# Kernel tuning notes

Hardware: AMD Instinct MI355X
Metric: run time of the kernel (lower is better)

The kernel has to match this reference:

```python
import jax, jax.numpy as jnp
import numpy as np

B, NPG, DEG = 512, 128, 16          # graphs, nodes/graph, out-degree
N = B * NPG                          # 65536 nodes
E = N * DEG                          # 1048576 edges
IN_DIM, HID, HEADS = 11, 32, 4
K1 = int(np.ceil(0.8 * NPG))         # 103 nodes/graph after pool1
K2 = int(np.ceil(0.8 * K1))          # 83 nodes/graph after pool2


def gat_conv(x, src, dst, mask, W, a_s, a_d, b, n_nodes):
    # PyG GATConv (concat=True, add_self_loops=True, eval mode -> no dropout)
    xp = (x @ W).reshape(n_nodes, HEADS, HID)            # [N,H,C]
    as_ = jnp.einsum('nhc,hc->nh', xp, a_s)
    ad_ = jnp.einsum('nhc,hc->nh', xp, a_d)
    loop = jnp.arange(n_nodes)
    s = jnp.concatenate([src, loop])
    d = jnp.concatenate([dst, loop])
    m = jnp.concatenate([mask, jnp.ones(n_nodes, bool)])
    logit = jax.nn.leaky_relu(as_[s] + ad_[d], 0.2)      # [E+N,H]
    logit = jnp.where(m[:, None], logit, -1e9)
    mx = jax.ops.segment_max(logit, d, num_segments=n_nodes)
    ex = jnp.exp(logit - mx[d]) * m[:, None]
    den = jax.ops.segment_sum(ex, d, num_segments=n_nodes)
    alpha = ex / (den[d] + 1e-16)                        # segment softmax over dst
    out = jax.ops.segment_sum(alpha[:, :, None] * xp[s], d, num_segments=n_nodes)
    return out.reshape(n_nodes, HEADS * HID) + b


def topk_pool(x, src, dst, mask, w, npg, k):
    # PyG TopKPooling: score = tanh((x*w).sum(-1)/||w||); keep top ceil(ratio*n) per graph
    nb = x.shape[0] // npg
    score = jnp.tanh((x @ w) / jnp.linalg.norm(w))
    vals, idx = jax.lax.top_k(score.reshape(nb, npg), k)  # [B,k]
    perm = (idx + (jnp.arange(nb) * npg)[:, None]).reshape(-1)
    x_new = x[perm] * vals.reshape(-1, 1)
    remap = jnp.full(nb * npg, -1).at[perm].set(jnp.arange(nb * k))
    ns, nd = remap[src], remap[dst]
    m = mask & (ns >= 0) & (nd >= 0)
    return x_new, jnp.where(m, ns, 0), jnp.where(m, nd, 0), m


def setup_inputs():
    key = jax.random.key(0)
    ks = jax.random.split(key, 24)
    s = 0.05
    x = jax.random.normal(ks[0], (N, IN_DIM), jnp.float32)
    src = jnp.repeat(jnp.arange(N), DEG)
    dst = (src // NPG) * NPG + jax.random.randint(ks[1], (E,), 0, NPG)
    edge_index = jnp.stack([src, dst])
    edge_attr = jax.random.normal(ks[2], (E, 4), jnp.float32)
    batch = jnp.repeat(jnp.arange(B), NPG)
    p = dict(
        W_g1=jax.random.normal(ks[3], (IN_DIM, HEADS * HID), jnp.float32) * s,
        att_src1=jax.random.normal(ks[4], (HEADS, HID), jnp.float32) * s,
        att_dst1=jax.random.normal(ks[5], (HEADS, HID), jnp.float32) * s,
        b_g1=jnp.zeros((HEADS * HID,), jnp.float32),
        W_t1=jax.random.normal(ks[6], (HEADS * HID, HID), jnp.float32) * s,
        b_t1=jnp.zeros((HID,), jnp.float32),
        pool_w1=jax.random.normal(ks[7], (HID,), jnp.float32) * s,
        W_g2=jax.random.normal(ks[8], (HID, HEADS * HID), jnp.float32) * s,
        att_src2=jax.random.normal(ks[9], (HEADS, HID), jnp.float32) * s,
        att_dst2=jax.random.normal(ks[10], (HEADS, HID), jnp.float32) * s,
        b_g2=jnp.zeros((HEADS * HID,), jnp.float32),
        W_t2=jax.random.normal(ks[11], (HEADS * HID, HID), jnp.float32) * s,
        b_t2=jnp.zeros((HID,), jnp.float32),
        pool_w2=jax.random.normal(ks[12], (HID,), jnp.float32) * s,
        W_l1=jax.random.normal(ks[13], (2 * HID, 256), jnp.float32) * s,
        b_l1=jnp.zeros((256,), jnp.float32),
        W_l2=jax.random.normal(ks[14], (256, 1024), jnp.float32) * s,
        b_l2=jnp.zeros((1024,), jnp.float32),
        W_l3=jax.random.normal(ks[15], (1024, 1), jnp.float32) * s,
        b_l3=jnp.zeros((1,), jnp.float32),
    )
    return dict(x=x, edge_index=edge_index, edge_attr=edge_attr, batch=batch, **p)


def reference(x, edge_index, edge_attr, batch,
              W_g1, att_src1, att_dst1, b_g1, W_t1, b_t1, pool_w1,
              W_g2, att_src2, att_dst2, b_g2, W_t2, b_t2, pool_w2,
              W_l1, b_l1, W_l2, b_l2, W_l3, b_l3):
    # edge_attr is ignored (GATConv built without edge_dim); batch is implicit
    # in the fixed equal-size graph layout.  Eval mode -> dropout disabled.
    src, dst = edge_index[0], edge_index[1]
    mask = jnp.ones(E, bool)
    h = jax.nn.relu(gat_conv(x, src, dst, mask, W_g1, att_src1, att_dst1, b_g1, N))
    h = h @ W_t1 + b_t1
    h, src, dst, mask = topk_pool(h, src, dst, mask, pool_w1, NPG, K1)
    h1 = h.reshape(B, K1, HID)
    g1 = jnp.concatenate([h1.max(1), h1.mean(1)], axis=1)   # [B, 2*HID]
    h = jax.nn.relu(gat_conv(h, src, dst, mask, W_g2, att_src2, att_dst2, b_g2, B * K1))
    h = h @ W_t2 + b_t2
    h, src, dst, mask = topk_pool(h, src, dst, mask, pool_w2, K1, K2)
    h2 = h.reshape(B, K2, HID)
    g2 = jnp.concatenate([h2.max(1), h2.mean(1)], axis=1)
    g = g1 + g2
    g = jax.nn.relu(g @ W_l1 + b_l1)
    g = jax.nn.relu(g @ W_l2 + b_l2)
    return g @ W_l3 + b_l3                                   # [B,1]
```

## Files before the change

kernel.cpp:

```cpp
#include <hip/hip_runtime.h>
#include <math.h>

constexpr int NPGc  = 128;
constexpr int NG    = 512;
constexpr int EPGc  = 2048;
constexpr int ETOT  = 1048576;
constexpr int IND   = 11;
constexpr int HIDc  = 32;
constexpr int FD    = 128;
constexpr int K1c   = 103;
constexpr int K2c   = 83;
constexpr int NN    = NG * NPGc;
constexpr int N2c   = NG * K1c;

__device__ __forceinline__ float lrelu(float x){ return fmaxf(x, 0.2f*x); }

__device__ __forceinline__ unsigned flipF(float f){
    unsigned u = __float_as_uint(f);
    return u ^ (unsigned)(((int)u >> 31) | 0x80000000);
}
__device__ __forceinline__ float unflipF(unsigned u){
    unsigned m = ((u >> 31) - 1u) | 0x80000000u;
    return __uint_as_float(u ^ m);
}

template<int KIN>
__device__ void foldDev(const float* __restrict__ Wg, const float* __restrict__ avs,
                        const float* __restrict__ avd, float* __restrict__ S, float* __restrict__ D, int t)
{
    if (t < KIN * 4) {
        int k = t >> 2, h = t & 3;
        float s = 0.f, d = 0.f;
        for (int j = 0; j < HIDc; j++) {
            float w = Wg[k*FD + h*HIDc + j];
            s = fmaf(w, avs[h*HIDc + j], s);
            d = fmaf(w, avd[h*HIDc + j], d);
        }
        S[t] = s; D[t] = d;
    }
}
__global__ void k_fold2(const float* W1, const float* s1, const float* d1, float* S1, float* D1,
                        const float* W2, const float* s2, const float* d2, float* S2, float* D2)
{
    if (blockIdx.x == 0) foldDev<IND>(W1, s1, d1, S1, D1, threadIdx.x);
    else                 foldDev<HIDc>(W2, s2, d2, S2, D2, threadIdx.x);
}

template<int NNODE, int KIN, bool REMAP>
__global__ __launch_bounds__(256) void k_gat(
    const float* __restrict__ xin, const float* __restrict__ Wg,
    const float* __restrict__ WsS, const float* __restrict__ WsD,
    const int* __restrict__ ei, const int* __restrict__ rankv,
    const float* __restrict__ bias, float* __restrict__ outp)
{
    int g = blockIdx.x, h = blockIdx.y, t = threadIdx.x;
    __shared__ __align__(16) float xpL[NNODE * 36];
    __shared__ float wE[EPGc];
    __shared__ unsigned char bucket[EPGc];
    __shared__ float asL[NNODE], adL[NNODE], mLn[NNODE], selfW[NNODE], sDen[NNODE];
    __shared__ unsigned maxAsU[NNODE];
    __shared__ int cnt[128], offA[130], curA[128];
    __shared__ float WL[KIN * 32];
    __shared__ float WsSL[KIN], WsDL[KIN];
    __shared__ float bL[32];
    __shared__ signed char rmap[NPGc];

    constexpr bool STAGE = (NNODE * KIN <= EPGc);
    float* xL = wE;

    for (int i = t; i < KIN * 32; i += 256) { int k = i >> 5, c = i & 31; WL[i] = Wg[k*FD + h*32 + c]; }
    if (t < KIN) { WsSL[t] = WsS[t*4 + h]; WsDL[t] = WsD[t*4 + h]; }
    if (t < 32) bL[t] = bias[h*32 + t];
    if (t < 128) cnt[t] = 0;
    if constexpr (REMAP) { if (t < NPGc) rmap[t] = (signed char)rankv[g*NPGc + t]; }
    if constexpr (STAGE) {
        const float* xg = xin + (size_t)g * NNODE * KIN;
        for (int i = t; i < NNODE * KIN; i += 256) xL[i] = xg[i];
    }
    __syncthreads();

    for (int p = t; p < NNODE * 32; p += 256) {
        int n = p >> 5, c = p & 31;
        float acc = 0.f;
        if constexpr (STAGE) {
            const float* xr = xL + n * KIN;
            #pragma unroll
            for (int k = 0; k < KIN; k++) acc = fmaf(xr[k], WL[k*32 + c], acc);
        } else {
            const float* xr = xin + (size_t)(g * NNODE + n) * KIN;
            #pragma unroll
            for (int k = 0; k < KIN; k++) acc = fmaf(xr[k], WL[k*32 + c], acc);
        }
        xpL[n*36 + c] = acc;
    }
    for (int n = t; n < NNODE; n += 256) {
        float s = 0.f, d = 0.f;
        if constexpr (STAGE) {
            const float* xr = xL + n * KIN;
            #pragma unroll
            for (int k = 0; k < KIN; k++) { float xv = xr[k]; s = fmaf(xv, WsSL[k], s); d = fmaf(xv, WsDL[k], d); }
        } else {
            const float* xr = xin + (size_t)(g * NNODE + n) * KIN;
            #pragma unroll
            for (int k = 0; k < KIN; k++) { float xv = xr[k]; s = fmaf(xv, WsSL[k], s); d = fmaf(xv, WsDL[k], d); }
        }
        asL[n] = s; adL[n] = d; maxAsU[n] = flipF(s);
    }
    __syncthreads();

    const int* dstG = ei + ETOT + g * EPGc;
    for (int e = t; e < EPGc; e += 256) {
        int dO = dstG[e] - g * NPGc, s0 = e >> 4;
        if constexpr (REMAP) {
            int sn = rmap[s0], dn = rmap[dO];
            if (sn >= 0 && dn >= 0) { atomicAdd(&cnt[dn], 1); atomicMax(&maxAsU[dn], flipF(asL[sn])); }
        } else {
            atomicAdd(&cnt[dO], 1); atomicMax(&maxAsU[dO], flipF(asL[s0]));
        }
    }
    __syncthreads();

    if (t < 64) {
        int c0 = cnt[2*t], c1 = cnt[2*t + 1], ps = c0 + c1, P = ps;
        #pragma unroll
        for (int dlt = 1; dlt < 64; dlt <<= 1) { int v = __shfl_up(P, dlt); if (t >= dlt) P += v; }
        int E0 = P - ps;
        offA[2*t] = E0; offA[2*t + 1] = E0 + c0;
        curA[2*t] = E0; curA[2*t + 1] = E0 + c0;
        if (t == 63) offA[128] = P;
    } else if (t < 64 + NNODE) {
        int n = t - 64;
        float m = lrelu(unflipF(maxAsU[n]) + adL[n]);
        mLn[n] = m;
        float ws = expf(lrelu(asL[n] + adL[n]) - m);
        selfW[n] = ws; sDen[n] = ws;
    }
    __syncthreads();

    for (int e = t; e < EPGc; e += 256) {
        int dO = dstG[e] - g * NPGc, s0 = e >> 4;
        int sn, dn; bool ok;
        if constexpr (REMAP) { sn = rmap[s0]; dn = rmap[dO]; ok = (sn >= 0 && dn >= 0); }
        else                 { sn = s0; dn = dO; ok = true; }
        if (ok) {
            float w = expf(lrelu(asL[sn] + adL[dn]) - mLn[dn]);
            int pos = atomicAdd(&curA[dn], 1);
            bucket[pos] = (unsigned char)sn; wE[pos] = w;
            atomicAdd(&sDen[dn], w);
        }
    }
    __syncthreads();

    const float4* X4 = (const float4*)xpL;
    for (int p = t; p < NNODE * 8; p += 256) {
        int n = p >> 3, c4 = p & 7;
        float w0 = selfW[n];
        float4 v = X4[n*9 + c4];
        float4 acc; acc.x = w0*v.x; acc.y = w0*v.y; acc.z = w0*v.z; acc.w = w0*v.w;
        int lo = offA[n], hi = offA[n + 1];
        for (int i = lo; i < hi; i++) {
            int sc = bucket[i]; float w = wE[i];
            float4 u = X4[sc*9 + c4];
            acc.x = fmaf(w, u.x, acc.x); acc.y = fmaf(w, u.y, acc.y);
            acc.z = fmaf(w, u.z, acc.z); acc.w = fmaf(w, u.w, acc.w);
        }
        float inv = 1.f / (sDen[n] + 1e-16f);
        float4 r;
        r.x = fmaxf(fmaf(acc.x, inv, bL[c4*4 + 0]), 0.f);
        r.y = fmaxf(fmaf(acc.y, inv, bL[c4*4 + 1]), 0.f);
        r.z = fmaxf(fmaf(acc.z, inv, bL[c4*4 + 2]), 0.f);
        r.w = fmaxf(fmaf(acc.w, inv, bL[c4*4 + 3]), 0.f);
        *(float4*)(outp + (size_t)(g * NNODE + n) * FD + h*32 + c4*4) = r;
    }
}

template<int NIN, int KEEP, bool FIRST>
__global__ __launch_bounds__(256) void k_linpool(
    const float* __restrict__ hg, const float* __restrict__ Wt, const float* __restrict__ bt,
    const float* __restrict__ pw, float* __restrict__ xnew, int* __restrict__ rankv,
    float* __restrict__ gfeat, const float* __restrict__ gprev)
{
    int g = blockIdx.x, t = threadIdx.x;
    __shared__ __align__(16) float hgT[NIN * 16];
    __shared__ float htL[NIN * 33];
    __shared__ float scoreL[NIN], valL[NIN];
    __shared__ int rnkL[NIN];

    int j = t & 31, nb = t >> 5;
    constexpr int RMAX = (NIN + 7) / 8;
    float acc[RMAX];
    float btj = bt[j];
    #pragma unroll
    for (int r = 0; r < RMAX; r++) acc[r] = btj;

    for (int kc = 0; kc < 8; kc++) {
        __syncthreads();
        for (int i = t; i < NIN * 4; i += 256) {
            int n = i >> 2, q = i & 3;
            ((float4*)hgT)[i] = *(const float4*)(hg + ((size_t)(g*NIN + n)*FD + kc*16 + q*4));
        }
        __syncthreads();
        float w[16];
        #pragma unroll
        for (int kk = 0; kk < 16; kk++) w[kk] = Wt[(kc*16 + kk)*HIDc + j];
        #pragma unroll
        for (int r = 0; r < RMAX; r++) {
            int n = nb + r*8; if (n >= NIN) break;
            const float4* hr = (const float4*)(hgT + n*16);
            float4 h0 = hr[0], h1 = hr[1], h2 = hr[2], h3 = hr[3];
            float a = acc[r];
            a = fmaf(h0.x, w[0],  a); a = fmaf(h0.y, w[1],  a); a = fmaf(h0.z, w[2],  a); a = fmaf(h0.w, w[3],  a);
            a = fmaf(h1.x, w[4],  a); a = fmaf(h1.y, w[5],  a); a = fmaf(h1.z, w[6],  a); a = fmaf(h1.w, w[7],  a);
            a = fmaf(h2.x, w[8],  a); a = fmaf(h2.y, w[9],  a); a = fmaf(h2.z, w[10], a); a = fmaf(h2.w, w[11], a);
            a = fmaf(h3.x, w[12], a); a = fmaf(h3.y, w[13], a); a = fmaf(h3.z, w[14], a); a = fmaf(h3.w, w[15], a);
            acc[r] = a;
        }
    }
    #pragma unroll
    for (int r = 0; r < RMAX; r++) { int n = nb + r*8; if (n < NIN) htL[n*33 + j] = acc[r]; }
    __syncthreads();

    float nrm; { float ss = 0.f; for (int k = 0; k < HIDc; k++) { float w = pw[k]; ss = fmaf(w, w, ss); } nrm = sqrtf(ss); }
    if (t < NIN) {
        float dot = 0.f;
        for (int k = 0; k < HIDc; k++) dot = fmaf(htL[t*33 + k], pw[k], dot);
        float val = tanhf(dot / nrm);
        scoreL[t] = val; valL[t] = val;
    }
    __syncthreads();
    if (t < NIN) {
        float si = scoreL[t]; int rank = 0;
        for (int q = 0; q < NIN; q++) {
            float sj = scoreL[q];
            rank += (sj > si || (sj == si && q < t)) ? 1 : 0;
        }
        rnkL[t] = (rank < KEEP) ? rank : -1;
    }
    __syncthreads();
    if (FIRST && t < NIN) rankv[g*NPGc + t] = rnkL[t];
    if (FIRST) {
        for (int p = t; p < NIN * 32; p += 256) {
            int n = p >> 5, jj = p & 31;
            int rk = rnkL[n];
            if (rk >= 0) xnew[((size_t)g*KEEP + rk)*HIDc + jj] = htL[n*33 + jj] * valL[n];
        }
    }
    if (t < HIDc) {
        float mx = -INFINITY, sm = 0.f;
        for (int n = 0; n < NIN; n++) {
            if (rnkL[n] >= 0) { float v = htL[n*33 + t] * valL[n]; mx = fmaxf(mx, v); sm += v; }
        }
        float mean = sm / (float)KEEP;
        if (FIRST) {
            gfeat[(size_t)g*64 + t] = mx;
            gfeat[(size_t)g*64 + 32 + t] = mean;
        } else {
            gfeat[(size_t)g*64 + t]      = gprev[(size_t)g*64 + t] + mx;
            gfeat[(size_t)g*64 + 32 + t] = gprev[(size_t)g*64 + 32 + t] + mean;
        }
    }
}

__global__ __launch_bounds__(256) void k_mlpA(const float* __restrict__ gsum,
    const float* __restrict__ W1, const float* __restrict__ b1,
    const float* __restrict__ W2, const float* __restrict__ b2,
    const float* __restrict__ W3, float* __restrict__ part)
{
    int gb = blockIdx.x, q = blockIdx.y, t = threadIdx.x;
    int g0 = gb * 4;
    __shared__ float gL[256];
    __shared__ float h1L[1024];
    __shared__ float4 red[256];
    gL[t] = gsum[(size_t)g0*64 + t];
    __syncthreads();
    float bv = b1[t];
    float a0 = bv, a1 = bv, a2 = bv, a3 = bv;
    #pragma unroll 4
    for (int k = 0; k < 64; k++) {
        float w = W1[k*256 + t];
        a0 = fmaf(gL[k], w, a0); a1 = fmaf(gL[64 + k], w, a1);
        a2 = fmaf(gL[128 + k], w, a2); a3 = fmaf(gL[192 + k], w, a3);
    }
    h1L[t] = fmaxf(a0, 0.f); h1L[256 + t] = fmaxf(a1, 0.f);
    h1L[512 + t] = fmaxf(a2, 0.f); h1L[768 + t] = fmaxf(a3, 0.f);
    __syncthreads();
    int o = q * 256 + t;
    float b2v = b2[o], w3 = W3[o];
    float c0 = b2v, c1 = b2v, c2 = b2v, c3 = b2v;
    const float* w2c = W2 + o;
    #pragma unroll 8
    for (int i = 0; i < 256; i++) {
        float w = w2c[(size_t)i * 1024];
        c0 = fmaf(h1L[i], w, c0); c1 = fmaf(h1L[256 + i], w, c1);
        c2 = fmaf(h1L[512 + i], w, c2); c3 = fmaf(h1L[768 + i], w, c3);
    }
    red[t] = make_float4(fmaxf(c0, 0.f)*w3, fmaxf(c1, 0.f)*w3, fmaxf(c2, 0.f)*w3, fmaxf(c3, 0.f)*w3);
    __syncthreads();
    for (int s = 128; s > 0; s >>= 1) {
        if (t < s) { float4 a = red[t], b = red[t + s]; a.x += b.x; a.y += b.y; a.z += b.z; a.w += b.w; red[t] = a; }
        __syncthreads();
    }
    if (t == 0) {
        float4 r = red[0];
        part[(size_t)(g0 + 0)*4 + q] = r.x;
        part[(size_t)(g0 + 1)*4 + q] = r.y;
        part[(size_t)(g0 + 2)*4 + q] = r.z;
        part[(size_t)(g0 + 3)*4 + q] = r.w;
    }
}

__global__ void k_mlpB(const float* __restrict__ part, const float* __restrict__ b3,
                       float* __restrict__ outp)
{
    int g = blockIdx.x * 256 + threadIdx.x;
    if (g < NG) {
        float4 p = ((const float4*)part)[g];
        outp[g] = ((p.x + p.y) + (p.z + p.w)) + b3[0];
    }
}

extern "C" void kernel_launch(void* const* d_in, const int* in_sizes, int n_in,
                              void* d_out, int out_size, void* d_ws, size_t ws_size,
                              hipStream_t stream)
{
    const float* x    = (const float*)d_in[0];
    const int*   ei   = (const int*)  d_in[1];
    const float* W_g1 = (const float*)d_in[4];
    const float* as1w = (const float*)d_in[5];
    const float* ad1w = (const float*)d_in[6];
    const float* b_g1 = (const float*)d_in[7];
    const float* W_t1 = (const float*)d_in[8];
    const float* b_t1 = (const float*)d_in[9];
    const float* pw1  = (const float*)d_in[10];
    const float* W_g2 = (const float*)d_in[11];
    const float* as2w = (const float*)d_in[12];
    const float* ad2w = (const float*)d_in[13];
    const float* b_g2 = (const float*)d_in[14];
    const float* W_t2 = (const float*)d_in[15];
    const float* b_t2 = (const float*)d_in[16];
    const float* pw2  = (const float*)d_in[17];
    const float* W_l1 = (const float*)d_in[18];
    const float* b_l1 = (const float*)d_in[19];
    const float* W_l2 = (const float*)d_in[20];
    const float* b_l2 = (const float*)d_in[21];
    const float* W_l3 = (const float*)d_in[22];
    const float* b_l3 = (const float*)d_in[23];
    float* out = (float*)d_out;

    char* ws = (char*)d_ws;
    size_t off = 0;
    auto alloc = [&](size_t elems) -> float* {
        float* p = (float*)(ws + off);
        off += ((elems * 4 + 255) / 256) * 256;
        return p;
    };
    float* hg1  = alloc((size_t)NN * FD);
    float* hg2  = alloc((size_t)N2c * FD);
    float* x2   = alloc((size_t)N2c * HIDc);
    int*   rank1= (int*)alloc((size_t)NN);
    float* g1   = alloc((size_t)NG * 64);
    float* gsum = alloc((size_t)NG * 64);
    float* part = alloc((size_t)NG * 4);
    float* wsS1 = alloc(64);
    float* wsD1 = alloc(64);
    float* wsS2 = alloc(128);
    float* wsD2 = alloc(128);

    k_fold2<<<2, 128, 0, stream>>>(W_g1, as1w, ad1w, wsS1, wsD1,
                                   W_g2, as2w, ad2w, wsS2, wsD2);

    k_gat<NPGc, IND, false><<<dim3(NG, 4), 256, 0, stream>>>(
        x, W_g1, wsS1, wsD1, ei, nullptr, b_g1, hg1);
    k_linpool<NPGc, K1c, true><<<NG, 256, 0, stream>>>(
        hg1, W_t1, b_t1, pw1, x2, rank1, g1, nullptr);

    k_gat<K1c, HIDc, true><<<dim3(NG, 4), 256, 0, stream>>>(
        x2, W_g2, wsS2, wsD2, ei, rank1, b_g2, hg2);
    k_linpool<K1c, K2c, false><<<NG, 256, 0, stream>>>(
        hg2, W_t2, b_t2, pw2, nullptr, nullptr, gsum, g1);

    k_mlpA<<<dim3(NG/4, 4), 256, 0, stream>>>(gsum, W_l1, b_l1, W_l2, b_l2, W_l3, part);
    k_mlpB<<<2, 256, 0, stream>>>(part, b_l3, out);
}
```

Baseline: 336.1 us.

## Split linear from pooling, drop fold kernel, recompute edge weights in aggregation

Removes the separate attention-fold kernel and computes per-node source and destination attention scores from the projected features in shared memory with a shuffle reduction. Edge indices are cached in registers between the count and bucket passes. Edge weights are no longer stored but recomputed with expf during aggregation. The fused linear-plus-pool kernel is split into a row-tiled linear kernel and a pool kernel, and workspace buffers are reused between the two layers. This trades extra exp work and an additional launch plus a global intermediate for lower shared memory use and better parallelism in the linear step.

```diff
diff --git a/kernel.cpp b/kernel.cpp
--- a/kernel.cpp
+++ b/kernel.cpp
@@ -24,98 +24,82 @@
     return __uint_as_float(u ^ m);
 }
 
-template<int KIN>
-__device__ void foldDev(const float* __restrict__ Wg, const float* __restrict__ avs,
-                        const float* __restrict__ avd, float* __restrict__ S, float* __restrict__ D, int t)
-{
-    if (t < KIN * 4) {
-        int k = t >> 2, h = t & 3;
-        float s = 0.f, d = 0.f;
-        for (int j = 0; j < HIDc; j++) {
-            float w = Wg[k*FD + h*HIDc + j];
-            s = fmaf(w, avs[h*HIDc + j], s);
-            d = fmaf(w, avd[h*HIDc + j], d);
-        }
-        S[t] = s; D[t] = d;
-    }
-}
-__global__ void k_fold2(const float* W1, const float* s1, const float* d1, float* S1, float* D1,
-                        const float* W2, const float* s2, const float* d2, float* S2, float* D2)
-{
-    if (blockIdx.x == 0) foldDev<IND>(W1, s1, d1, S1, D1, threadIdx.x);
-    else                 foldDev<HIDc>(W2, s2, d2, S2, D2, threadIdx.x);
-}
-
 template<int NNODE, int KIN, bool REMAP>
 __global__ __launch_bounds__(256) void k_gat(
     const float* __restrict__ xin, const float* __restrict__ Wg,
-    const float* __restrict__ WsS, const float* __restrict__ WsD,
+    const float* __restrict__ avs, const float* __restrict__ avd,
     const int* __restrict__ ei, const int* __restrict__ rankv,
     const float* __restrict__ bias, float* __restrict__ outp)
 {
     int g = blockIdx.x, h = blockIdx.y, t = threadIdx.x;
     __shared__ __align__(16) float xpL[NNODE * 36];
-    __shared__ float wE[EPGc];
+    __shared__ __align__(16) float xF[NNODE * KIN];
     __shared__ unsigned char bucket[EPGc];
-    __shared__ float asL[NNODE], adL[NNODE], mLn[NNODE], selfW[NNODE], sDen[NNODE];
+    __shared__ float asL[NNODE], adL[NNODE], sDen[NNODE];
     __shared__ unsigned maxAsU[NNODE];
-    __shared__ int cnt[128], offA[130], curA[128];
+    __shared__ int cnt[128], offA[129], curA[128];
     __shared__ float WL[KIN * 32];
-    __shared__ float WsSL[KIN], WsDL[KIN];
-    __shared__ float bL[32];
-    __shared__ signed char rmap[NPGc];
-
-    constexpr bool STAGE = (NNODE * KIN <= EPGc);
-    float* xL = wE;
-
+    __shared__ float avsL[32], avdL[32], bL[32];
+    __shared__ signed char rmap[REMAP ? NPGc : 1];
+
+    float* mLn = (float*)maxAsU;
+
+    {
+        const float* xg = xin + (size_t)g * NNODE * KIN;
+        if constexpr ((KIN & 3) == 0) {
+            for (int i = t; i < NNODE * (KIN/4); i += 256)
+                ((float4*)xF)[i] = ((const float4*)xg)[i];
+        } else {
+            for (int i = t; i < NNODE * KIN; i += 256) xF[i] = xg[i];
+        }
+    }
     for (int i = t; i < KIN * 32; i += 256) { int k = i >> 5, c = i & 31; WL[i] = Wg[k*FD + h*32 + c]; }
-    if (t < KIN) { WsSL[t] = WsS[t*4 + h]; WsDL[t] = WsD[t*4 + h]; }
-    if (t < 32) bL[t] = bias[h*32 + t];
+    if (t < 32) { avsL[t] = avs[h*32 + t]; avdL[t] = avd[h*32 + t]; bL[t] = bias[h*32 + t]; }
     if (t < 128) cnt[t] = 0;
     if constexpr (REMAP) { if (t < NPGc) rmap[t] = (signed char)rankv[g*NPGc + t]; }
-    if constexpr (STAGE) {
-        const float* xg = xin + (size_t)g * NNODE * KIN;
-        for (int i = t; i < NNODE * KIN; i += 256) xL[i] = xg[i];
-    }
     __syncthreads();
 
     for (int p = t; p < NNODE * 32; p += 256) {
         int n = p >> 5, c = p & 31;
+        const float* xr = xF + n * KIN;
         float acc = 0.f;
-        if constexpr (STAGE) {
-            const float* xr = xL + n * KIN;
-            #pragma unroll
-            for (int k = 0; k < KIN; k++) acc = fmaf(xr[k], WL[k*32 + c], acc);
-        } else {
-            const float* xr = xin + (size_t)(g * NNODE + n) * KIN;
-            #pragma unroll
-            for (int k = 0; k < KIN; k++) acc = fmaf(xr[k], WL[k*32 + c], acc);
-        }
+        #pragma unroll
+        for (int k = 0; k < KIN; k++) acc = fmaf(xr[k], WL[k*32 + c], acc);
         xpL[n*36 + c] = acc;
     }
-    for (int n = t; n < NNODE; n += 256) {
+    __syncthreads();
+
+    for (int p = t; p < NNODE * 8; p += 256) {
+        int n = p >> 3, jo = p & 7;
+        const float* xr = xpL + n*36 + jo*4;
         float s = 0.f, d = 0.f;
-        if constexpr (STAGE) {
-            const float* xr = xL + n * KIN;
-            #pragma unroll
-            for (int k = 0; k < KIN; k++) { float xv = xr[k]; s = fmaf(xv, WsSL[k], s); d = fmaf(xv, WsDL[k], d); }
-        } else {
-            const float* xr = xin + (size_t)(g * NNODE + n) * KIN;
-            #pragma unroll
-            for (int k = 0; k < KIN; k++) { float xv = xr[k]; s = fmaf(xv, WsSL[k], s); d = fmaf(xv, WsDL[k], d); }
-        }
-        asL[n] = s; adL[n] = d; maxAsU[n] = flipF(s);
+        #pragma unroll
+        for (int jj = 0; jj < 4; jj++) {
+            float v = xr[jj];
+            s = fmaf(v, avsL[jo*4 + jj], s);
+            d = fmaf(v, avdL[jo*4 + jj], d);
+        }
+        s += __shfl_xor(s, 1); d += __shfl_xor(d, 1);
+        s += __shfl_xor(s, 2); d += __shfl_xor(d, 2);
+        s += __shfl_xor(s, 4); d += __shfl_xor(d, 4);
+        if (jo == 0) { asL[n] = s; adL[n] = d; maxAsU[n] = flipF(s); }
     }
     __syncthreads();
 
     const int* dstG = ei + ETOT + g * EPGc;
-    for (int e = t; e < EPGc; e += 256) {
+    int snR[8], dnR[8];
+    #pragma unroll
+    for (int q = 0; q < 8; q++) {
+        int e = t + 256*q;
         int dO = dstG[e] - g * NPGc, s0 = e >> 4;
         if constexpr (REMAP) {
             int sn = rmap[s0], dn = rmap[dO];
-            if (sn >= 0 && dn >= 0) { atomicAdd(&cnt[dn], 1); atomicMax(&maxAsU[dn], flipF(asL[sn])); }
-        } else {
-            atomicAdd(&cnt[dO], 1); atomicMax(&maxAsU[dO], flipF(asL[s0]));
+            bool ok = (sn >= 0 && dn >= 0);
+            snR[q] = ok ? sn : -1; dnR[q] = ok ? dn : -1;
+        } else { snR[q] = s0; dnR[q] = dO; }
+        if (dnR[q] >= 0) {
+            atomicAdd(&cnt[dnR[q]], 1);
+            atomicMax(&maxAsU[dnR[q]], flipF(asL[snR[q]]));
         }
     }
     __syncthreads();
@@ -131,21 +115,20 @@
     } else if (t < 64 + NNODE) {
         int n = t - 64;
         float m = lrelu(unflipF(maxAsU[n]) + adL[n]);
+        float ws = expf(lrelu(asL[n] + adL[n]) - m);
+        sDen[n] = ws;
         mLn[n] = m;
-        float ws = expf(lrelu(asL[n] + adL[n]) - m);
-        selfW[n] = ws; sDen[n] = ws;
-    }
-    __syncthreads();
-
-    for (int e = t; e < EPGc; e += 256) {
-        int dO = dstG[e] - g * NPGc, s0 = e >> 4;
-        int sn, dn; bool ok;
-        if constexpr (REMAP) { sn = rmap[s0]; dn = rmap[dO]; ok = (sn >= 0 && dn >= 0); }
-        else                 { sn = s0; dn = dO; ok = true; }
-        if (ok) {
+    }
+    __syncthreads();
+
+    #pragma unroll
+    for (int q = 0; q < 8; q++) {
+        int dn = dnR[q];
+        if (dn >= 0) {
+            int sn = snR[q];
             float w = expf(lrelu(asL[sn] + adL[dn]) - mLn[dn]);
             int pos = atomicAdd(&curA[dn], 1);
-            bucket[pos] = (unsigned char)sn; wE[pos] = w;
+            bucket[pos] = (unsigned char)sn;
             atomicAdd(&sDen[dn], w);
         }
     }
@@ -154,12 +137,14 @@
     const float4* X4 = (const float4*)xpL;
     for (int p = t; p < NNODE * 8; p += 256) {
         int n = p >> 3, c4 = p & 7;
-        float w0 = selfW[n];
+        float adn = adL[n], m = mLn[n];
+        float w0 = expf(lrelu(asL[n] + adn) - m);
         float4 v = X4[n*9 + c4];
         float4 acc; acc.x = w0*v.x; acc.y = w0*v.y; acc.z = w0*v.z; acc.w = w0*v.w;
         int lo = offA[n], hi = offA[n + 1];
         for (int i = lo; i < hi; i++) {
-            int sc = bucket[i]; float w = wE[i];
+            int sc = bucket[i];
+            float w = expf(lrelu(asL[sc] + adn) - m);
             float4 u = X4[sc*9 + c4];
             acc.x = fmaf(w, u.x, acc.x); acc.y = fmaf(w, u.y, acc.y);
             acc.z = fmaf(w, u.z, acc.z); acc.w = fmaf(w, u.w, acc.w);
@@ -174,52 +159,50 @@
     }
 }
 
+__global__ __launch_bounds__(256) void k_lin(const float* __restrict__ in,
+    const float* __restrict__ W, const float* __restrict__ b, float* __restrict__ outp)
+{
+    __shared__ float WtL[FD * HIDc];
+    int t = threadIdx.x;
+    for (int i = t; i < FD * HIDc; i += 256) WtL[i] = W[i];
+    __syncthreads();
+    int j = t & 31, rg = t >> 5;
+    int r0 = blockIdx.x * 32 + rg * 4;
+    const float* i0 = in + (size_t)r0 * FD;
+    float bj = b[j];
+    float a0 = bj, a1 = bj, a2 = bj, a3 = bj;
+    for (int k4 = 0; k4 < 32; k4++) {
+        float4 v0 = *(const float4*)(i0 + k4*4);
+        float4 v1 = *(const float4*)(i0 + FD + k4*4);
+        float4 v2 = *(const float4*)(i0 + 2*FD + k4*4);
+        float4 v3 = *(const float4*)(i0 + 3*FD + k4*4);
+        float w0 = WtL[(k4*4 + 0)*HIDc + j], w1 = WtL[(k4*4 + 1)*HIDc + j];
+        float w2 = WtL[(k4*4 + 2)*HIDc + j], w3 = WtL[(k4*4 + 3)*HIDc + j];
+        a0 = fmaf(v0.x, w0, a0); a0 = fmaf(v0.y, w1, a0); a0 = fmaf(v0.z, w2, a0); a0 = fmaf(v0.w, w3, a0);
+        a1 = fmaf(v1.x, w0, a1); a1 = fmaf(v1.y, w1, a1); a1 = fmaf(v1.z, w2, a1); a1 = fmaf(v1.w, w3, a1);
+        a2 = fmaf(v2.x, w0, a2); a2 = fmaf(v2.y, w1, a2); a2 = fmaf(v2.z, w2, a2); a2 = fmaf(v2.w, w3, a2);
+        a3 = fmaf(v3.x, w0, a3); a3 = fmaf(v3.y, w1, a3); a3 = fmaf(v3.z, w2, a3); a3 = fmaf(v3.w, w3, a3);
+    }
+    size_t ob = (size_t)r0 * HIDc + j;
+    outp[ob] = a0; outp[ob + 32] = a1; outp[ob + 64] = a2; outp[ob + 96] = a3;
+}
+
 template<int NIN, int KEEP, bool FIRST>
-__global__ __launch_bounds__(256) void k_linpool(
-    const float* __restrict__ hg, const float* __restrict__ Wt, const float* __restrict__ bt,
+__global__ __launch_bounds__(256) void k_pool(const float* __restrict__ ht,
     const float* __restrict__ pw, float* __restrict__ xnew, int* __restrict__ rankv,
     float* __restrict__ gfeat, const float* __restrict__ gprev)
 {
     int g = blockIdx.x, t = threadIdx.x;
-    __shared__ __align__(16) float hgT[NIN * 16];
     __shared__ float htL[NIN * 33];
     __shared__ float scoreL[NIN], valL[NIN];
     __shared__ int rnkL[NIN];
-
-    int j = t & 31, nb = t >> 5;
-    constexpr int RMAX = (NIN + 7) / 8;
-    float acc[RMAX];
-    float btj = bt[j];
-    #pragma unroll
-    for (int r = 0; r < RMAX; r++) acc[r] = btj;
-
-    for (int kc = 0; kc < 8; kc++) {
-        __syncthreads();
-        for (int i = t; i < NIN * 4; i += 256) {
-            int n = i >> 2, q = i & 3;
-            ((float4*)hgT)[i] = *(const float4*)(hg + ((size_t)(g*NIN + n)*FD + kc*16 + q*4));
-        }
-        __syncthreads();
-        float w[16];
-        #pragma unroll
-        for (int kk = 0; kk < 16; kk++) w[kk] = Wt[(kc*16 + kk)*HIDc + j];
-        #pragma unroll
-        for (int r = 0; r < RMAX; r++) {
-            int n = nb + r*8; if (n >= NIN) break;
-            const float4* hr = (const float4*)(hgT + n*16);
-            float4 h0 = hr[0], h1 = hr[1], h2 = hr[2], h3 = hr[3];
-            float a = acc[r];
-            a = fmaf(h0.x, w[0],  a); a = fmaf(h0.y, w[1],  a); a = fmaf(h0.z, w[2],  a); a = fmaf(h0.w, w[3],  a);
-            a = fmaf(h1.x, w[4],  a); a = fmaf(h1.y, w[5],  a); a = fmaf(h1.z, w[6],  a); a = fmaf(h1.w, w[7],  a);
-            a = fmaf(h2.x, w[8],  a); a = fmaf(h2.y, w[9],  a); a = fmaf(h2.z, w[10], a); a = fmaf(h2.w, w[11], a);
-            a = fmaf(h3.x, w[12], a); a = fmaf(h3.y, w[13], a); a = fmaf(h3.z, w[14], a); a = fmaf(h3.w, w[15], a);
-            acc[r] = a;
-        }
-    }
-    #pragma unroll
-    for (int r = 0; r < RMAX; r++) { int n = nb + r*8; if (n < NIN) htL[n*33 + j] = acc[r]; }
-    __syncthreads();
-
+    for (int i = t; i < NIN * 8; i += 256) {
+        int n = i >> 3, q = i & 7;
+        float4 v = *(const float4*)(ht + (size_t)(g*NIN + n)*HIDc + q*4);
+        float* dst = htL + n*33 + q*4;
+        dst[0] = v.x; dst[1] = v.y; dst[2] = v.z; dst[3] = v.w;
+    }
+    __syncthreads();
     float nrm; { float ss = 0.f; for (int k = 0; k < HIDc; k++) { float w = pw[k]; ss = fmaf(w, w, ss); } nrm = sqrtf(ss); }
     if (t < NIN) {
         float dot = 0.f;
@@ -235,9 +218,9 @@
             rank += (sj > si || (sj == si && q < t)) ? 1 : 0;
         }
         rnkL[t] = (rank < KEEP) ? rank : -1;
-    }
-    __syncthreads();
-    if (FIRST && t < NIN) rankv[g*NPGc + t] = rnkL[t];
+        if (FIRST) rankv[g*NPGc + t] = rnkL[t];
+    }
+    __syncthreads();
     if (FIRST) {
         for (int p = t; p < NIN * 32; p += 256) {
             int n = p >> 5, jj = p & 31;
@@ -252,7 +235,7 @@
         }
         float mean = sm / (float)KEEP;
         if (FIRST) {
-            gfeat[(size_t)g*64 + t] = mx;
+            gfeat[(size_t)g*64 + t]      = mx;
             gfeat[(size_t)g*64 + 32 + t] = mean;
         } else {
             gfeat[(size_t)g*64 + t]      = gprev[(size_t)g*64 + t] + mx;
@@ -355,29 +338,26 @@
         return p;
     };
     float* hg1  = alloc((size_t)NN * FD);
-    float* hg2  = alloc((size_t)N2c * FD);
+    float* ht1  = alloc((size_t)NN * HIDc);
     float* x2   = alloc((size_t)N2c * HIDc);
     int*   rank1= (int*)alloc((size_t)NN);
     float* g1   = alloc((size_t)NG * 64);
     float* gsum = alloc((size_t)NG * 64);
     float* part = alloc((size_t)NG * 4);
-    float* wsS1 = alloc(64);
-    float* wsD1 = alloc(64);
-    float* wsS2 = alloc(128);
-    float* wsD2 = alloc(128);
-
-    k_fold2<<<2, 128, 0, stream>>>(W_g1, as1w, ad1w, wsS1, wsD1,
-                                   W_g2, as2w, ad2w, wsS2, wsD2);
+    float* hg2 = hg1;
+    float* ht2 = ht1;
 
     k_gat<NPGc, IND, false><<<dim3(NG, 4), 256, 0, stream>>>(
-        x, W_g1, wsS1, wsD1, ei, nullptr, b_g1, hg1);
-    k_linpool<NPGc, K1c, true><<<NG, 256, 0, stream>>>(
-        hg1, W_t1, b_t1, pw1, x2, rank1, g1, nullptr);
+        x, W_g1, as1w, ad1w, ei, nullptr, b_g1, hg1);
+    k_lin<<<NN/32, 256, 0, stream>>>(hg1, W_t1, b_t1, ht1);
+    k_pool<NPGc, K1c, true><<<NG, 256, 0, stream>>>(
+        ht1, pw1, x2, rank1, g1, nullptr);
 
     k_gat<K1c, HIDc, true><<<dim3(NG, 4), 256, 0, stream>>>(
-        x2, W_g2, wsS2, wsD2, ei, rank1, b_g2, hg2);
-    k_linpool<K1c, K2c, false><<<NG, 256, 0, stream>>>(
-        hg2, W_t2, b_t2, pw2, nullptr, nullptr, gsum, g1);
+        x2, W_g2, as2w, ad2w, ei, rank1, b_g2, hg2);
+    k_lin<<<N2c/32, 256, 0, stream>>>(hg2, W_t2, b_t2, ht2);
+    k_pool<K1c, K2c, false><<<NG, 256, 0, stream>>>(
+        ht2, pw2, nullptr, nullptr, gsum, g1);
 
     k_mlpA<<<dim3(NG/4, 4), 256, 0, stream>>>(gsum, W_l1, b_l1, W_l2, b_l2, W_l3, part);
     k_mlpB<<<2, 256, 0, stream>>>(part, b_l3, out);
```

After: 365.0 us. 8.6% more time.
